# Kernel tuning notes

Hardware: AMD Instinct MI355X
Metric: run time of the kernel (lower is better)

Reference implementation:

```python
import jax, jax.numpy as jnp
import numpy as np

# Last adaptive-conv stage of AdaBIGGAN (BigGAN-128): ch=96 at 128x128, hypernet input dim 148
B, C, H, W, IN = 32, 96, 128, 128, 148


def setup_inputs() -> dict:
    key = jax.random.key(0)
    k0, k1, k2, k3, k4, k5 = jax.random.split(key, 6)
    s = 0.02  # small init scale for hypernetwork linears
    return {
        "h": jax.random.normal(k0, (B, C, H, W), jnp.float32),      # feature map after cond-BN
        "y": jax.random.normal(k1, (B, IN), jnp.float32),           # [shared_embed | z-chunk] cond vector
        "Wg_w": jax.random.normal(k2, (C * C, IN), jnp.float32) * s,  # nn.Linear(148, C*C).weight
        "Wg_b": jax.random.normal(k3, (C * C,), jnp.float32) * s,     # nn.Linear(148, C*C).bias
        "Bg_w": jax.random.normal(k4, (C, IN), jnp.float32) * s,      # nn.Linear(148, C).weight
        "Bg_b": jax.random.normal(k5, (C,), jnp.float32) * s,         # nn.Linear(148, C).bias
    }


def reference(h, y, Wg_w, Wg_b, Bg_w, Bg_b):
    Bn, Cn = h.shape[0], h.shape[1]
    # hypernetwork: per-sample 1x1-conv weight [B, C, C] and bias [B, C]
    w = (y @ Wg_w.T + Wg_b).reshape(Bn, Cn, Cn)
    b = y @ Bg_w.T + Bg_b
    # Faithful to the torch broadcasting: (h[:, :, None] * w[:, :, :, None, None]).sum(2)
    # which collapses exactly to h * w.sum(-1), avoiding the [B,C,C,H,W] blowup.
    scale = w.sum(-1)  # [B, C]
    out = h * scale[:, :, None, None] + b[:, :, None, None]
    return jax.nn.relu(out)  # block.activation1
```

## Files before the change

kernel.cpp:

```cpp
#include <hip/hip_runtime.h>
#include <stdint.h>

#define B_  32
#define C_  96
#define HW_ 16384
#define IN_ 148

__global__ __launch_bounds__(256) void hyper_kernel(
    const float* __restrict__ Wg_w, const float* __restrict__ Wg_b,
    const float* __restrict__ Bg_w, const float* __restrict__ Bg_b,
    const float* __restrict__ y,
    float* __restrict__ scale, float* __restrict__ bias) {
    const int c   = blockIdx.x;
    const int tid = threadIdx.x;

    __shared__ float sW[IN_];
    __shared__ float sB[IN_];
    __shared__ float sWbS;

    if (tid < IN_) {
        float s = 0.f;
        const float* p = Wg_w + (size_t)c * C_ * IN_ + tid;
        #pragma unroll 4
        for (int j = 0; j < C_; ++j) s += p[(size_t)j * IN_];
        sW[tid] = s;
        sB[tid] = Bg_w[c * IN_ + tid];
    }
    if (tid < 64) {
        float v = Wg_b[c * C_ + tid];
        if (tid < C_ - 64) v += Wg_b[c * C_ + 64 + tid];
        #pragma unroll
        for (int off = 32; off > 0; off >>= 1) v += __shfl_down(v, off);
        if (tid == 0) sWbS = v;
    }
    __syncthreads();

    const int wave = tid >> 6, lane = tid & 63;
    for (int b = wave; b < B_; b += 4) {
        float y0 = y[b * IN_ + lane];
        float y1 = y[b * IN_ + 64 + lane];
        float ps = y0 * sW[lane] + y1 * sW[64 + lane];
        float pb = y0 * sB[lane] + y1 * sB[64 + lane];
        if (lane < IN_ - 128) {
            float y2 = y[b * IN_ + 128 + lane];
            ps += y2 * sW[128 + lane];
            pb += y2 * sB[128 + lane];
        }
        #pragma unroll
        for (int off = 32; off > 0; off >>= 1) {
            ps += __shfl_down(ps, off);
            pb += __shfl_down(pb, off);
        }
        if (lane == 0) {
            scale[b * C_ + c] = ps + sWbS;
            bias [b * C_ + c] = pb + Bg_b[c];
        }
    }
}

__global__ __launch_bounds__(256) void apply_kernel(
    const float* __restrict__ h, const float* __restrict__ scale,
    const float* __restrict__ bias, float* __restrict__ out) {
    const int idx   = blockIdx.x * 256 + threadIdx.x;
    const int plane = idx >> 12;

    const float s  = scale[plane];
    const float bb = bias[plane];

    const float4 v = reinterpret_cast<const float4*>(h)[idx];
    float4 o;
    o.x = fmaxf(fmaf(v.x, s, bb), 0.f);
    o.y = fmaxf(fmaf(v.y, s, bb), 0.f);
    o.z = fmaxf(fmaf(v.z, s, bb), 0.f);
    o.w = fmaxf(fmaf(v.w, s, bb), 0.f);
    reinterpret_cast<float4*>(out)[idx] = o;
}

extern "C" void kernel_launch(void* const* d_in, const int* in_sizes, int n_in,
                              void* d_out, int out_size, void* d_ws, size_t ws_size,
                              hipStream_t stream) {
    const float* h    = (const float*)d_in[0];
    const float* y    = (const float*)d_in[1];
    const float* Wg_w = (const float*)d_in[2];
    const float* Wg_b = (const float*)d_in[3];
    const float* Bg_w = (const float*)d_in[4];
    const float* Bg_b = (const float*)d_in[5];
    float* out = (float*)d_out;

    float* scale = (float*)d_ws;
    float* bias  = scale + B_ * C_;

    hyper_kernel<<<C_, 256, 0, stream>>>(Wg_w, Wg_b, Bg_w, Bg_b, y, scale, bias);

    const int nvec = (B_ * C_ * HW_) / 4;
    apply_kernel<<<nvec / 256, 256, 0, stream>>>(h, scale, bias, out);
}
```

Baseline: 347.5 us.

## Use nontemporal 2x-vector loads/stores in apply and split hypernet column sums

```diff
diff --git a/kernel.cpp b/kernel.cpp
--- a/kernel.cpp
+++ b/kernel.cpp
@@ -6,7 +6,9 @@
 #define HW_ 16384
 #define IN_ 148
 
-__global__ __launch_bounds__(256) void hyper_kernel(
+typedef float f32x4 __attribute__((ext_vector_type(4)));
+
+__global__ __launch_bounds__(512) void hyper_kernel(
     const float* __restrict__ Wg_w, const float* __restrict__ Wg_b,
     const float* __restrict__ Bg_w, const float* __restrict__ Bg_b,
     const float* __restrict__ y,
@@ -14,17 +16,20 @@
     const int c   = blockIdx.x;
     const int tid = threadIdx.x;
 
+    __shared__ float sW2[2][IN_];
     __shared__ float sW[IN_];
     __shared__ float sB[IN_];
     __shared__ float sWbS;
 
-    if (tid < IN_) {
+    if (tid < 2 * IN_) {
+        const int half = (tid >= IN_) ? 1 : 0;
+        const int col  = tid - half * IN_;
+        const float* p = Wg_w + (size_t)c * C_ * IN_ + (size_t)(half * 48) * IN_ + col;
         float s = 0.f;
-        const float* p = Wg_w + (size_t)c * C_ * IN_ + tid;
         #pragma unroll 4
-        for (int j = 0; j < C_; ++j) s += p[(size_t)j * IN_];
-        sW[tid] = s;
-        sB[tid] = Bg_w[c * IN_ + tid];
+        for (int j = 0; j < 48; ++j) s += p[(size_t)j * IN_];
+        sW2[half][col] = s;
+        if (half == 0) sB[col] = Bg_w[c * IN_ + col];
     }
     if (tid < 64) {
         float v = Wg_b[c * C_ + tid];
@@ -34,9 +39,11 @@
         if (tid == 0) sWbS = v;
     }
     __syncthreads();
+    if (tid < IN_) sW[tid] = sW2[0][tid] + sW2[1][tid];
+    __syncthreads();
 
     const int wave = tid >> 6, lane = tid & 63;
-    for (int b = wave; b < B_; b += 4) {
+    for (int b = wave; b < B_; b += 8) {
         float y0 = y[b * IN_ + lane];
         float y1 = y[b * IN_ + 64 + lane];
         float ps = y0 * sW[lane] + y1 * sW[64 + lane];
@@ -61,19 +68,25 @@
 __global__ __launch_bounds__(256) void apply_kernel(
     const float* __restrict__ h, const float* __restrict__ scale,
     const float* __restrict__ bias, float* __restrict__ out) {
-    const int idx   = blockIdx.x * 256 + threadIdx.x;
-    const int plane = idx >> 12;
+    const int cidx  = blockIdx.x * 256 + threadIdx.x;
+    const int plane = cidx >> 11;
 
     const float s  = scale[plane];
     const float bb = bias[plane];
 
-    const float4 v = reinterpret_cast<const float4*>(h)[idx];
-    float4 o;
-    o.x = fmaxf(fmaf(v.x, s, bb), 0.f);
-    o.y = fmaxf(fmaf(v.y, s, bb), 0.f);
-    o.z = fmaxf(fmaf(v.z, s, bb), 0.f);
-    o.w = fmaxf(fmaf(v.w, s, bb), 0.f);
-    reinterpret_cast<float4*>(out)[idx] = o;
+    const f32x4* hp = reinterpret_cast<const f32x4*>(h) + (size_t)cidx * 2;
+    f32x4*       op = reinterpret_cast<f32x4*>(out)     + (size_t)cidx * 2;
+
+    f32x4 v0 = __builtin_nontemporal_load(hp);
+    f32x4 v1 = __builtin_nontemporal_load(hp + 1);
+    f32x4 o0, o1;
+    #pragma unroll
+    for (int k = 0; k < 4; ++k) {
+        o0[k] = fmaxf(fmaf(v0[k], s, bb), 0.f);
+        o1[k] = fmaxf(fmaf(v1[k], s, bb), 0.f);
+    }
+    __builtin_nontemporal_store(o0, op);
+    __builtin_nontemporal_store(o1, op + 1);
 }
 
 extern "C" void kernel_launch(void* const* d_in, const int* in_sizes, int n_in,
@@ -90,8 +103,8 @@
     float* scale = (float*)d_ws;
     float* bias  = scale + B_ * C_;
 
-    hyper_kernel<<<C_, 256, 0, stream>>>(Wg_w, Wg_b, Bg_w, Bg_b, y, scale, bias);
+    hyper_kernel<<<C_, 512, 0, stream>>>(Wg_w, Wg_b, Bg_w, Bg_b, y, scale, bias);
 
-    const int nvec = (B_ * C_ * HW_) / 4;
-    apply_kernel<<<nvec / 256, 256, 0, stream>>>(h, scale, bias, out);
+    const int nchunk = (B_ * C_ * HW_) / 8;
+    apply_kernel<<<nchunk / 256, 256, 0, stream>>>(h, scale, bias, out);
 }
```

After: 348.9 us. Within noise of the previous version (+0.4%).
